# Kernel optimization log

Measured on AMD Instinct MI355X. Metric: run time of the kernel, lower is better.

## Reference

```python
import jax, jax.numpy as jnp
import numpy as np

B, M, N, Z = 4, 64, 64, 64
IN_DIM, OUT_DIM = 32, 32
MODES1 = MODES2 = MODES3 = 16
HIDDEN = OUT_DIM * 4  # factor=4, n_ff_layers=2
LN_EPS = 1e-5


def setup_inputs() -> dict:
    key = jax.random.key(0)
    ks = jax.random.split(key, 10)
    # xavier-normal-ish scale for (in, out, modes, 2) fourier weights
    fscale = np.sqrt(2.0 / (IN_DIM + OUT_DIM))
    x = jax.random.normal(ks[0], (B, M, N, Z, IN_DIM), dtype=jnp.float32)
    wx = jax.random.normal(ks[1], (IN_DIM, OUT_DIM, MODES1, 2), dtype=jnp.float32) * fscale
    wy = jax.random.normal(ks[2], (IN_DIM, OUT_DIM, MODES2, 2), dtype=jnp.float32) * fscale
    wz = jax.random.normal(ks[3], (IN_DIM, OUT_DIM, MODES3, 2), dtype=jnp.float32) * fscale
    # FeedForward: Linear(OUT_DIM, HIDDEN) + ReLU, then Linear(HIDDEN, OUT_DIM) + LayerNorm
    w0 = jax.random.normal(ks[4], (OUT_DIM, HIDDEN), dtype=jnp.float32) * np.sqrt(1.0 / OUT_DIM)
    b0 = jnp.zeros((HIDDEN,), dtype=jnp.float32)
    w1 = jax.random.normal(ks[5], (HIDDEN, OUT_DIM), dtype=jnp.float32) * np.sqrt(1.0 / HIDDEN)
    b1 = jnp.zeros((OUT_DIM,), dtype=jnp.float32)
    ln_g = jnp.ones((OUT_DIM,), dtype=jnp.float32)
    ln_b = jnp.zeros((OUT_DIM,), dtype=jnp.float32)
    return {"x": x, "wx": wx, "wy": wy, "wz": wz,
            "w0": w0, "b0": b0, "w1": w1, "b1": b1,
            "ln_g": ln_g, "ln_b": ln_b}


def _as_complex(w):
    return w[..., 0] + 1j * w[..., 1]


def _forward_fourier(x, wx, wy, wz):
    # x: [b, m, n, z, i] -> [b, i, m, n, z]
    xt = jnp.transpose(x, (0, 4, 1, 2, 3))
    # --- axis M (dim 2) ---
    ftx = jnp.fft.rfft(xt, axis=2, norm='ortho')  # [b, i, M//2+1, n, z] complex
    ox = jnp.einsum('bixyz,iox->boxyz', ftx[:, :, :MODES1], _as_complex(wx))
    ox = jnp.pad(ox, ((0, 0), (0, 0), (0, M // 2 + 1 - MODES1), (0, 0), (0, 0)))
    xx = jnp.fft.irfft(ox, n=M, axis=2, norm='ortho')
    # --- axis N (dim 3) ---
    fty = jnp.fft.rfft(xt, axis=3, norm='ortho')
    oy = jnp.einsum('bixyz,ioy->boxyz', fty[:, :, :, :MODES2], _as_complex(wy))
    oy = jnp.pad(oy, ((0, 0), (0, 0), (0, 0), (0, N // 2 + 1 - MODES2), (0, 0)))
    xy = jnp.fft.irfft(oy, n=N, axis=3, norm='ortho')
    # --- axis Z (dim 4) ---
    ftz = jnp.fft.rfft(xt, axis=4, norm='ortho')
    oz = jnp.einsum('bixyz,ioz->boxyz', ftz[:, :, :, :, :MODES3], _as_complex(wz))
    oz = jnp.pad(oz, ((0, 0), (0, 0), (0, 0), (0, 0), (0, Z // 2 + 1 - MODES3)))
    xz = jnp.fft.irfft(oz, n=Z, axis=4, norm='ortho')
    out = xx + xy + xz  # [b, o, m, n, z]
    return jnp.transpose(out, (0, 2, 3, 4, 1))  # [b, m, n, z, o]


def reference(x, wx, wy, wz, w0, b0, w1, b1, ln_g, ln_b):
    s = _forward_fourier(x, wx, wy, wz)
    h = jax.nn.relu(s @ w0 + b0)
    y = h @ w1 + b1
    mu = jnp.mean(y, axis=-1, keepdims=True)
    var = jnp.mean((y - mu) ** 2, axis=-1, keepdims=True)
    y = (y - mu) * jax.lax.rsqrt(var + LN_EPS) * ln_g + ln_b
    return y
```

## Files before the change

### kernel.cpp

```cpp
#include <hip/hip_runtime.h>
#include <math.h>

typedef __attribute__((ext_vector_type(8))) short short8v;
typedef __attribute__((ext_vector_type(4))) float float4v;

constexpr float THETA = 6.28318530717958647692f / 64.0f;

constexpr int S_B = 64 * 64 * 64 * 32;
constexpr int S_M = 64 * 64 * 32;
constexpr int S_N = 64 * 32;
constexpr int S_Z = 32;

__device__ __forceinline__ unsigned short f2bf(float f) {
    unsigned int u = __builtin_bit_cast(unsigned int, f);
    u += 0x7FFFu + ((u >> 16) & 1u);
    return (unsigned short)(u >> 16);
}
__device__ __forceinline__ float bf2f(unsigned int h) {
    return __builtin_bit_cast(float, h << 16);
}

constexpr int WS_TF = 98304, WS_TI = 100352, WS_TOTAL = 102400;

__global__ __launch_bounds__(256)
void setup_frags(const float* __restrict__ wx, const float* __restrict__ wy,
                 const float* __restrict__ wz, unsigned short* __restrict__ W)
{
    int f0 = (blockIdx.x * 256 + threadIdx.x) * 4;
#pragma unroll
    for (int u = 0; u < 4; ++u) {
        int f = f0 + u;
        if (f >= WS_TOTAL) continue;
        unsigned short v;
        if (f < WS_TF) {
            int ax = f >> 15, rem = f & 32767;
            int k = rem >> 11;
            int rem2 = rem & 2047;
            int wt = rem2 >> 10, rt = (rem2 >> 9) & 1, l = (rem2 >> 3) & 63, e = rem2 & 7;
            int o = 16 * rt + (l & 15), i = 8 * (l >> 4) + e;
            const float* w = (ax == 0) ? wx : ((ax == 1) ? wy : wz);
            v = f2bf(w[((i * 32 + o) * 16 + k) * 2 + wt]);
        } else if (f < WS_TI) {
            int rem = f - WS_TF;
            int jt = rem >> 10, s = (rem >> 9) & 1, l = (rem >> 3) & 63, e = rem & 7;
            int kk = l & 15, m = 32 * s + 8 * (l >> 4) + e;
            int jm = (kk * m) & 63;
            float ang = THETA * (float)jm;
            v = f2bf(jt == 0 ? cosf(ang) : sinf(ang));
        } else {
            int rem = f - WS_TI;
            int mt = rem >> 9, l = (rem >> 3) & 63, e = rem & 7;
            int mp = 16 * mt + (l & 15), r = 8 * (l >> 4) + e;
            int k = r & 15;
            float sk = (k == 0) ? (1.0f / 64.0f) : (2.0f / 64.0f);
            int jm = (k * mp) & 63;
            float ang = THETA * (float)jm;
            v = f2bf(r < 16 ? sk * cosf(ang) : -sk * sinf(ang));
        }
        W[f] = v;
    }
}

constexpr int AB_SHORTS = 4096;
__device__ __forceinline__ int ab4(int t, int k, int line, int i) {
    return ((((t * 16 + k) * 4 + line) * 64) + i * 2) ^ (((line ^ k) & 7) << 4);
}
constexpr int P_LS = 1288;
constexpr int P_SHORTS = 4 * P_LS;
__device__ __forceinline__ int p4(int line, int o, int r) {
    return line * P_LS + o * 40 + r;
}

template <int STRIDE>
__device__ __forceinline__ void stageF1(const float* __restrict__ x, long bs,
                                        const unsigned short* __restrict__ tf,
                                        unsigned short* __restrict__ AB,
                                        int lane, int line)
{
    const int gq = lane >> 4, c = lane & 15;
    short8v tfB[2][2];
#pragma unroll
    for (int jt = 0; jt < 2; ++jt)
#pragma unroll
        for (int s = 0; s < 2; ++s)
            tfB[jt][s] = *reinterpret_cast<const short8v*>(tf + ((jt * 2 + s) * 64 + lane) * 8);

    float4v acc[2][2];
#pragma unroll
    for (int rt = 0; rt < 2; ++rt)
#pragma unroll
        for (int jt = 0; jt < 2; ++jt)
            acc[rt][jt] = float4v{0.f, 0.f, 0.f, 0.f};

#pragma unroll
    for (int rt = 0; rt < 2; ++rt) {
        const float* xp = x + bs + 16 * rt + c;
#pragma unroll
        for (int s = 0; s < 2; ++s) {
            short8v a;
#pragma unroll
            for (int e = 0; e < 8; ++e)
                a[e] = (short)f2bf(xp[(long)(32 * s + 8 * gq + e) * STRIDE]);
            acc[rt][0] = __builtin_amdgcn_mfma_f32_16x16x32_bf16(a, tfB[0][s], acc[rt][0], 0, 0, 0);
            acc[rt][1] = __builtin_amdgcn_mfma_f32_16x16x32_bf16(a, tfB[1][s], acc[rt][1], 0, 0, 0);
        }
    }
#pragma unroll
    for (int rt = 0; rt < 2; ++rt)
#pragma unroll
        for (int jt = 0; jt < 2; ++jt) {
            unsigned int lo = (unsigned int)f2bf(acc[rt][jt][0]) | ((unsigned int)f2bf(acc[rt][jt][1]) << 16);
            unsigned int hi = (unsigned int)f2bf(acc[rt][jt][2]) | ((unsigned int)f2bf(acc[rt][jt][3]) << 16);
            *reinterpret_cast<uint2*>(reinterpret_cast<char*>(AB) + ab4(jt, c, line, 16 * rt + 4 * gq)) =
                make_uint2(lo, hi);
        }
}

__device__ __forceinline__ void stageMx4(const unsigned short* __restrict__ wf,
                                         const unsigned short* __restrict__ AB,
                                         unsigned short* __restrict__ P,
                                         int lane, int wave)
{
    const int gq = lane >> 4, c = lane & 15;
    const int t2 = wave >> 1, rt = wave & 1, lc = c & 3;
    for (int k = 0; k < 16; k += 2) {
        float4v acc2[2];
#pragma unroll
        for (int kk = 0; kk < 2; ++kk) {
            const int kc = k + kk;
            short8v aT = *reinterpret_cast<const short8v*>(reinterpret_cast<const char*>(AB) + ab4(0, kc, lc, 8 * gq));
            short8v bT = *reinterpret_cast<const short8v*>(reinterpret_cast<const char*>(AB) + ab4(1, kc, lc, 8 * gq));
            const int w1t = t2 ? 1 : 0, w2t = t2 ? 0 : 1;
            short8v w1 = *reinterpret_cast<const short8v*>(wf + (((kc * 2 + w1t) * 2 + rt) * 64 + lane) * 8);
            short8v w2 = *reinterpret_cast<const short8v*>(wf + (((kc * 2 + w2t) * 2 + rt) * 64 + lane) * 8);
            if (t2) {
                union { short8v s; unsigned int u[4]; } nb;
                nb.s = bT;
#pragma unroll
                for (int j = 0; j < 4; ++j) nb.u[j] ^= 0x80008000u;
                bT = nb.s;
            }
            float4v a2 = float4v{0.f, 0.f, 0.f, 0.f};
            a2 = __builtin_amdgcn_mfma_f32_16x16x32_bf16(w1, aT, a2, 0, 0, 0);
            a2 = __builtin_amdgcn_mfma_f32_16x16x32_bf16(w2, bT, a2, 0, 0, 0);
            acc2[kk] = a2;
        }
        if (c < 4) {
#pragma unroll
            for (int r = 0; r < 4; ++r) {
                unsigned int u = (unsigned int)f2bf(acc2[0][r]) | ((unsigned int)f2bf(acc2[1][r]) << 16);
                *reinterpret_cast<unsigned int*>(&P[p4(c, 16 * rt + 4 * gq + r, 16 * t2 + k)]) = u;
            }
        }
    }
}

template <int AXIS, int MODE>
__global__ __launch_bounds__(256)
void spectral_mfma(const float* __restrict__ x,
                   const unsigned short* __restrict__ wf,
                   const unsigned short* __restrict__ tf,
                   const unsigned short* __restrict__ ti,
                   float* __restrict__ out,
                   unsigned short* __restrict__ pw)
{
    __shared__ __align__(16) unsigned short AB[AB_SHORTS];
    __shared__ __align__(16) unsigned short P[P_SHORTS];

    const int t = threadIdx.x, lane = t & 63, wave = t >> 6;
    const int gq = lane >> 4, c = lane & 15;
    constexpr int stride = (AXIS == 0) ? S_M : S_N;

    const int l = blockIdx.x * 4 + wave;
    const int b = l >> 12, p1 = (l >> 6) & 63, p2 = l & 63;
    const long bs = (AXIS == 0)
        ? (long)b * S_B + (long)p1 * S_N + (long)p2 * S_Z
        : (long)b * S_B + (long)p1 * S_M + (long)p2 * S_Z;

    stageF1<stride>(x, bs, tf, AB, lane, wave);
    __syncthreads();
    stageMx4(wf, AB, P, lane, wave);
    __syncthreads();

    short8v tiB[4];
#pragma unroll
    for (int mt = 0; mt < 4; ++mt)
        tiB[mt] = *reinterpret_cast<const short8v*>(ti + (mt * 64 + lane) * 8);

    short8v pA[2];
    pA[0] = *reinterpret_cast<const short8v*>(&P[p4(wave, c, 8 * gq)]);
    pA[1] = *reinterpret_cast<const short8v*>(&P[p4(wave, 16 + c, 8 * gq)]);

#pragma unroll
    for (int rt = 0; rt < 2; ++rt)
#pragma unroll
        for (int mt = 0; mt < 4; ++mt) {
            float4v acc = float4v{0.f, 0.f, 0.f, 0.f};
            acc = __builtin_amdgcn_mfma_f32_16x16x32_bf16(pA[rt], tiB[mt], acc, 0, 0, 0);
            const long off = bs + (long)(16 * mt + c) * stride + 16 * rt + 4 * gq;
            if (MODE == 0) {
                *reinterpret_cast<float4*>(out + off) = make_float4(acc[0], acc[1], acc[2], acc[3]);
            } else if (MODE == 1) {
                float4 old = *reinterpret_cast<const float4*>(out + off);
                old.x += acc[0]; old.y += acc[1]; old.z += acc[2]; old.w += acc[3];
                *reinterpret_cast<float4*>(out + off) = old;
            } else if (MODE == 2) {
                uint2 pv;
                pv.x = (unsigned int)f2bf(acc[0]) | ((unsigned int)f2bf(acc[1]) << 16);
                pv.y = (unsigned int)f2bf(acc[2]) | ((unsigned int)f2bf(acc[3]) << 16);
                *reinterpret_cast<uint2*>(pw + off) = pv;
            } else {
                uint2 old = *reinterpret_cast<const uint2*>(pw + off);
                const float v0 = bf2f(old.x & 0xffffu) + acc[0];
                const float v1 = bf2f(old.x >> 16)     + acc[1];
                const float v2 = bf2f(old.y & 0xffffu) + acc[2];
                const float v3 = bf2f(old.y >> 16)     + acc[3];
                uint2 pv;
                pv.x = (unsigned int)f2bf(v0) | ((unsigned int)f2bf(v1) << 16);
                pv.y = (unsigned int)f2bf(v2) | ((unsigned int)f2bf(v3) << 16);
                *reinterpret_cast<uint2*>(pw + off) = pv;
            }
        }
}

template <bool BF16P>
__global__ __launch_bounds__(256)
void spectral_fused(const float* __restrict__ x,
                    const unsigned short* __restrict__ wf,
                    const unsigned short* __restrict__ tf,
                    const unsigned short* __restrict__ ti,
                    const float* __restrict__ w0, const float* __restrict__ b0,
                    const float* __restrict__ w1, const float* __restrict__ b1,
                    const float* __restrict__ g,  const float* __restrict__ bb,
                    const void* __restrict__ partial,
                    float* __restrict__ out)
{
    __shared__ __align__(16) unsigned short sm[23584];
    constexpr int OP = 8192, OS = 13344;

    const int t = threadIdx.x, lane = t & 63, wave = t >> 6;
    const int gq = lane >> 4, c = lane & 15;

    const int l = blockIdx.x * 4 + wave;
    const int b = l >> 12, p1 = (l >> 6) & 63, p2 = l & 63;
    const long bs = (long)b * S_B + (long)p1 * S_M + (long)p2 * S_N;

    float b0v[8], b1v[2], gv[2], bvv[2];
#pragma unroll
    for (int n = 0; n < 8; ++n) b0v[n] = b0[n * 16 + c];
#pragma unroll
    for (int n = 0; n < 2; ++n) { b1v[n] = b1[n * 16 + c]; gv[n] = g[n * 16 + c]; bvv[n] = bb[n * 16 + c]; }

    stageF1<S_Z>(x, bs, tf, sm, lane, wave);
    __syncthreads();
    stageMx4(wf, sm, sm + OP, lane, wave);
    __syncthreads();

    for (int s = t; s < 512; s += 256) {
        const int n = s >> 6, ln = s & 63, g2 = ln >> 4, c2 = ln & 15;
        const int kb = n >> 1, nn = n & 1;
        short8v v0, v1;
#pragma unroll
        for (int e = 0; e < 8; ++e) {
            v0[e] = (short)f2bf(w0[(8 * g2 + e) * 128 + n * 16 + c2]);
            v1[e] = (short)f2bf(w1[(32 * kb + 8 * g2 + e) * 32 + nn * 16 + c2]);
        }
        *reinterpret_cast<short8v*>(&sm[s * 8])        = v0;
        *reinterpret_cast<short8v*>(&sm[4096 + s * 8]) = v1;
    }

    short8v tiB[4];
#pragma unroll
    for (int mt = 0; mt < 4; ++mt)
        tiB[mt] = *reinterpret_cast<const short8v*>(ti + (mt * 64 + lane) * 8);

    {
        short8v pA[2];
        pA[0] = *reinterpret_cast<const short8v*>(&sm[OP + p4(wave, c, 8 * gq)]);
        pA[1] = *reinterpret_cast<const short8v*>(&sm[OP + p4(wave, 16 + c, 8 * gq)]);
#pragma unroll
        for (int rt = 0; rt < 2; ++rt)
#pragma unroll
            for (int mt = 0; mt < 4; ++mt) {
                float4v acc = float4v{0.f, 0.f, 0.f, 0.f};
                acc = __builtin_amdgcn_mfma_f32_16x16x32_bf16(pA[rt], tiB[mt], acc, 0, 0, 0);
                const long off = bs + (long)(16 * mt + c) * S_Z + 16 * rt + 4 * gq;
                float v0, v1, v2, v3;
                if (BF16P) {
                    uint2 pv = *reinterpret_cast<const uint2*>((const unsigned short*)partial + off);
                    v0 = bf2f(pv.x & 0xffffu) + acc[0];
                    v1 = bf2f(pv.x >> 16)     + acc[1];
                    v2 = bf2f(pv.y & 0xffffu) + acc[2];
                    v3 = bf2f(pv.y >> 16)     + acc[3];
                } else {
                    float4 old = *reinterpret_cast<const float4*>((const float*)partial + off);
                    v0 = old.x + acc[0]; v1 = old.y + acc[1];
                    v2 = old.z + acc[2]; v3 = old.w + acc[3];
                }
                const int si = OS + (wave * 64 + 16 * mt + c) * 40 + 16 * rt + 4 * gq;
                *reinterpret_cast<unsigned int*>(&sm[si])     = (unsigned int)f2bf(v0) | ((unsigned int)f2bf(v1) << 16);
                *reinterpret_cast<unsigned int*>(&sm[si + 2]) = (unsigned int)f2bf(v2) | ((unsigned int)f2bf(v3) << 16);
            }
    }
    __syncthreads();

    const int Hb = OS + wave * 2560;

    short8v af[4];
#pragma unroll
    for (int f = 0; f < 4; ++f)
        af[f] = *reinterpret_cast<const short8v*>(&sm[OS + (wave * 64 + 16 * f + c) * 40 + 8 * gq]);

    float4v Y[4][2];
#pragma unroll
    for (int f = 0; f < 4; ++f)
#pragma unroll
        for (int n = 0; n < 2; ++n)
            Y[f][n] = float4v{b1v[n], b1v[n], b1v[n], b1v[n]};

#pragma unroll
    for (int kb = 0; kb < 4; ++kb) {
#pragma unroll
        for (int nn = 0; nn < 2; ++nn) {
            const int n = 2 * kb + nn;
            const short8v wv = *reinterpret_cast<const short8v*>(&sm[(n * 64 + lane) * 8]);
#pragma unroll
            for (int f = 0; f < 4; ++f) {
                float4v hacc = float4v{b0v[n], b0v[n], b0v[n], b0v[n]};
                hacc = __builtin_amdgcn_mfma_f32_16x16x32_bf16(af[f], wv, hacc, 0, 0, 0);
#pragma unroll
                for (int r = 0; r < 4; ++r)
                    sm[Hb + (16 * f + 4 * gq + r) * 40 + nn * 16 + c] = f2bf(fmaxf(hacc[r], 0.f));
            }
        }
        const short8v wva = *reinterpret_cast<const short8v*>(&sm[4096 + ((kb * 2 + 0) * 64 + lane) * 8]);
        const short8v wvb = *reinterpret_cast<const short8v*>(&sm[4096 + ((kb * 2 + 1) * 64 + lane) * 8]);
#pragma unroll
        for (int f = 0; f < 4; ++f) {
            const short8v a2 = *reinterpret_cast<const short8v*>(&sm[Hb + (16 * f + c) * 40 + 8 * gq]);
            Y[f][0] = __builtin_amdgcn_mfma_f32_16x16x32_bf16(a2, wva, Y[f][0], 0, 0, 0);
            Y[f][1] = __builtin_amdgcn_mfma_f32_16x16x32_bf16(a2, wvb, Y[f][1], 0, 0, 0);
        }
    }

#pragma unroll
    for (int f = 0; f < 4; ++f) {
        float smv[4], sq[4];
#pragma unroll
        for (int r = 0; r < 4; ++r) {
            const float v0 = Y[f][0][r], v1 = Y[f][1][r];
            smv[r] = v0 + v1;
            sq[r]  = v0 * v0 + v1 * v1;
        }
#pragma unroll
        for (int mask = 1; mask <= 8; mask <<= 1) {
#pragma unroll
            for (int r = 0; r < 4; ++r) {
                smv[r] += __shfl_xor(smv[r], mask);
                sq[r]  += __shfl_xor(sq[r], mask);
            }
        }
#pragma unroll
        for (int r = 0; r < 4; ++r) {
            const float mu = smv[r] * (1.0f / 32.0f);
            const float var = sq[r] * (1.0f / 32.0f) - mu * mu;
            const float rs = rsqrtf(var + 1e-5f);
            float* op = out + bs + (long)(16 * f + 4 * gq + r) * 32;
            op[c]      = (Y[f][0][r] - mu) * rs * gv[0] + bvv[0];
            op[16 + c] = (Y[f][1][r] - mu) * rs * gv[1] + bvv[1];
        }
    }
}

extern "C" void kernel_launch(void* const* d_in, const int* in_sizes, int n_in,
                              void* d_out, int out_size, void* d_ws, size_t ws_size,
                              hipStream_t stream)
{
    const float* x    = (const float*)d_in[0];
    const float* wx   = (const float*)d_in[1];
    const float* wy   = (const float*)d_in[2];
    const float* wz   = (const float*)d_in[3];
    const float* w0   = (const float*)d_in[4];
    const float* b0   = (const float*)d_in[5];
    const float* w1   = (const float*)d_in[6];
    const float* b1   = (const float*)d_in[7];
    const float* ln_g = (const float*)d_in[8];
    const float* ln_b = (const float*)d_in[9];
    float* out = (float*)d_out;

    unsigned short* wsf = (unsigned short*)d_ws;

    const size_t PART_OFF   = 262144;
    const size_t PART_BYTES = (size_t)33554432 * 2;
    const bool bf16p = ws_size >= PART_OFF + PART_BYTES;
    unsigned short* pw = (unsigned short*)((char*)d_ws + PART_OFF);

    setup_frags<<<100, 256, 0, stream>>>(wx, wy, wz, wsf);

    if (bf16p) {
        spectral_mfma<0, 2><<<4096, 256, 0, stream>>>(x, wsf + 0 * 32768, wsf + WS_TF, wsf + WS_TI, out, pw);
        spectral_mfma<1, 3><<<4096, 256, 0, stream>>>(x, wsf + 1 * 32768, wsf + WS_TF, wsf + WS_TI, out, pw);
        spectral_fused<true><<<4096, 256, 0, stream>>>(x, wsf + 2 * 32768, wsf + WS_TF, wsf + WS_TI,
                                                       w0, b0, w1, b1, ln_g, ln_b, pw, out);
    } else {
        spectral_mfma<0, 0><<<4096, 256, 0, stream>>>(x, wsf + 0 * 32768, wsf + WS_TF, wsf + WS_TI, out, pw);
        spectral_mfma<1, 1><<<4096, 256, 0, stream>>>(x, wsf + 1 * 32768, wsf + WS_TF, wsf + WS_TI, out, pw);
        spectral_fused<false><<<4096, 256, 0, stream>>>(x, wsf + 2 * 32768, wsf + WS_TF, wsf + WS_TI,
                                                        w0, b0, w1, b1, ln_g, ln_b, out, out);
    }
}
```

Baseline: 229.1 us.

## Merge X and Y spectral passes into one launch with separate bf16 partial buffers

Adds a combined spectral_xy kernel that runs the M-axis and N-axis spectral passes as one 8192-block launch. Each pass writes its own bf16 partial buffer, which removes the read-modify-write accumulation of the second pass and lets both passes run concurrently. The fused Z/FFN kernel then reads and sums both partials. Smaller changes: bf16 conversion now uses the native __bf16 cast, and the first FFN matmul is transposed so each lane stores a packed uint2 instead of four scalar shared-memory writes. The new path needs twice the workspace for partials and falls back to the old paths otherwise.

```diff
diff --git a/kernel.cpp b/kernel.cpp
--- a/kernel.cpp
+++ b/kernel.cpp
@@ -12,9 +12,11 @@
 constexpr int S_Z = 32;
 
 __device__ __forceinline__ unsigned short f2bf(float f) {
-    unsigned int u = __builtin_bit_cast(unsigned int, f);
-    u += 0x7FFFu + ((u >> 16) & 1u);
-    return (unsigned short)(u >> 16);
+    __bf16 h = (__bf16)f;
+    return __builtin_bit_cast(unsigned short, h);
+}
+__device__ __forceinline__ unsigned int pkbf(float lo, float hi) {
+    return (unsigned int)f2bf(lo) | ((unsigned int)f2bf(hi) << 16);
 }
 __device__ __forceinline__ float bf2f(unsigned int h) {
     return __builtin_bit_cast(float, h << 16);
@@ -109,10 +111,8 @@
     for (int rt = 0; rt < 2; ++rt)
 #pragma unroll
         for (int jt = 0; jt < 2; ++jt) {
-            unsigned int lo = (unsigned int)f2bf(acc[rt][jt][0]) | ((unsigned int)f2bf(acc[rt][jt][1]) << 16);
-            unsigned int hi = (unsigned int)f2bf(acc[rt][jt][2]) | ((unsigned int)f2bf(acc[rt][jt][3]) << 16);
             *reinterpret_cast<uint2*>(reinterpret_cast<char*>(AB) + ab4(jt, c, line, 16 * rt + 4 * gq)) =
-                make_uint2(lo, hi);
+                make_uint2(pkbf(acc[rt][jt][0], acc[rt][jt][1]), pkbf(acc[rt][jt][2], acc[rt][jt][3]));
         }
 }
 
@@ -148,10 +148,72 @@
         if (c < 4) {
 #pragma unroll
             for (int r = 0; r < 4; ++r) {
-                unsigned int u = (unsigned int)f2bf(acc2[0][r]) | ((unsigned int)f2bf(acc2[1][r]) << 16);
-                *reinterpret_cast<unsigned int*>(&P[p4(c, 16 * rt + 4 * gq + r, 16 * t2 + k)]) = u;
-            }
-        }
+                *reinterpret_cast<unsigned int*>(&P[p4(c, 16 * rt + 4 * gq + r, 16 * t2 + k)]) =
+                    pkbf(acc2[0][r], acc2[1][r]);
+            }
+        }
+    }
+}
+
+template <int AXIS>
+__device__ __forceinline__ void spectral_body(const float* __restrict__ x,
+                                              const unsigned short* __restrict__ wf,
+                                              const unsigned short* __restrict__ tf,
+                                              const unsigned short* __restrict__ ti,
+                                              unsigned short* __restrict__ pw,
+                                              unsigned short* __restrict__ AB,
+                                              unsigned short* __restrict__ P,
+                                              int l, int lane, int wave)
+{
+    constexpr int stride = (AXIS == 0) ? S_M : S_N;
+    const int b = l >> 12, p1 = (l >> 6) & 63, p2 = l & 63;
+    const long bs = (AXIS == 0)
+        ? (long)b * S_B + (long)p1 * S_N + (long)p2 * S_Z
+        : (long)b * S_B + (long)p1 * S_M + (long)p2 * S_Z;
+    const int gq = lane >> 4, c = lane & 15;
+
+    stageF1<stride>(x, bs, tf, AB, lane, wave);
+    __syncthreads();
+    stageMx4(wf, AB, P, lane, wave);
+    __syncthreads();
+
+    short8v tiB[4];
+#pragma unroll
+    for (int mt = 0; mt < 4; ++mt)
+        tiB[mt] = *reinterpret_cast<const short8v*>(ti + (mt * 64 + lane) * 8);
+
+    short8v pA[2];
+    pA[0] = *reinterpret_cast<const short8v*>(&P[p4(wave, c, 8 * gq)]);
+    pA[1] = *reinterpret_cast<const short8v*>(&P[p4(wave, 16 + c, 8 * gq)]);
+
+#pragma unroll
+    for (int rt = 0; rt < 2; ++rt)
+#pragma unroll
+        for (int mt = 0; mt < 4; ++mt) {
+            float4v acc = float4v{0.f, 0.f, 0.f, 0.f};
+            acc = __builtin_amdgcn_mfma_f32_16x16x32_bf16(pA[rt], tiB[mt], acc, 0, 0, 0);
+            const long off = bs + (long)(16 * mt + c) * stride + 16 * rt + 4 * gq;
+            *reinterpret_cast<uint2*>(pw + off) =
+                make_uint2(pkbf(acc[0], acc[1]), pkbf(acc[2], acc[3]));
+        }
+}
+
+__global__ __launch_bounds__(256)
+void spectral_xy(const float* __restrict__ x,
+                 const unsigned short* __restrict__ wf0,
+                 const unsigned short* __restrict__ wf1,
+                 const unsigned short* __restrict__ tf,
+                 const unsigned short* __restrict__ ti,
+                 unsigned short* __restrict__ pw1,
+                 unsigned short* __restrict__ pw2)
+{
+    __shared__ __align__(16) unsigned short AB[AB_SHORTS];
+    __shared__ __align__(16) unsigned short P[P_SHORTS];
+    const int t = threadIdx.x, lane = t & 63, wave = t >> 6;
+    if (blockIdx.x < 4096) {
+        spectral_body<0>(x, wf0, tf, ti, pw1, AB, P, blockIdx.x * 4 + wave, lane, wave);
+    } else {
+        spectral_body<1>(x, wf1, tf, ti, pw2, AB, P, (blockIdx.x - 4096) * 4 + wave, lane, wave);
     }
 }
 
@@ -205,25 +267,21 @@
                 old.x += acc[0]; old.y += acc[1]; old.z += acc[2]; old.w += acc[3];
                 *reinterpret_cast<float4*>(out + off) = old;
             } else if (MODE == 2) {
-                uint2 pv;
-                pv.x = (unsigned int)f2bf(acc[0]) | ((unsigned int)f2bf(acc[1]) << 16);
-                pv.y = (unsigned int)f2bf(acc[2]) | ((unsigned int)f2bf(acc[3]) << 16);
-                *reinterpret_cast<uint2*>(pw + off) = pv;
+                *reinterpret_cast<uint2*>(pw + off) =
+                    make_uint2(pkbf(acc[0], acc[1]), pkbf(acc[2], acc[3]));
             } else {
                 uint2 old = *reinterpret_cast<const uint2*>(pw + off);
                 const float v0 = bf2f(old.x & 0xffffu) + acc[0];
                 const float v1 = bf2f(old.x >> 16)     + acc[1];
                 const float v2 = bf2f(old.y & 0xffffu) + acc[2];
                 const float v3 = bf2f(old.y >> 16)     + acc[3];
-                uint2 pv;
-                pv.x = (unsigned int)f2bf(v0) | ((unsigned int)f2bf(v1) << 16);
-                pv.y = (unsigned int)f2bf(v2) | ((unsigned int)f2bf(v3) << 16);
-                *reinterpret_cast<uint2*>(pw + off) = pv;
-            }
-        }
-}
-
-template <bool BF16P>
+                *reinterpret_cast<uint2*>(pw + off) =
+                    make_uint2(pkbf(v0, v1), pkbf(v2, v3));
+            }
+        }
+}
+
+template <int NPART>
 __global__ __launch_bounds__(256)
 void spectral_fused(const float* __restrict__ x,
                     const unsigned short* __restrict__ wf,
@@ -232,7 +290,9 @@
                     const float* __restrict__ w0, const float* __restrict__ b0,
                     const float* __restrict__ w1, const float* __restrict__ b1,
                     const float* __restrict__ g,  const float* __restrict__ bb,
-                    const void* __restrict__ partial,
+                    const unsigned short* __restrict__ pw1,
+                    const unsigned short* __restrict__ pw2,
+                    const float* __restrict__ pf32,
                     float* __restrict__ out)
 {
     __shared__ __align__(16) unsigned short sm[23584];
@@ -245,9 +305,11 @@
     const int b = l >> 12, p1 = (l >> 6) & 63, p2 = l & 63;
     const long bs = (long)b * S_B + (long)p1 * S_M + (long)p2 * S_N;
 
-    float b0v[8], b1v[2], gv[2], bvv[2];
-#pragma unroll
-    for (int n = 0; n < 8; ++n) b0v[n] = b0[n * 16 + c];
+    float4 b0q[8];
+#pragma unroll
+    for (int n = 0; n < 8; ++n)
+        b0q[n] = *reinterpret_cast<const float4*>(b0 + 16 * n + 4 * gq);
+    float b1v[2], gv[2], bvv[2];
 #pragma unroll
     for (int n = 0; n < 2; ++n) { b1v[n] = b1[n * 16 + c]; gv[n] = g[n * 16 + c]; bvv[n] = bb[n * 16 + c]; }
 
@@ -286,20 +348,26 @@
                 acc = __builtin_amdgcn_mfma_f32_16x16x32_bf16(pA[rt], tiB[mt], acc, 0, 0, 0);
                 const long off = bs + (long)(16 * mt + c) * S_Z + 16 * rt + 4 * gq;
                 float v0, v1, v2, v3;
-                if (BF16P) {
-                    uint2 pv = *reinterpret_cast<const uint2*>((const unsigned short*)partial + off);
+                if (NPART == 0) {
+                    float4 old = *reinterpret_cast<const float4*>(pf32 + off);
+                    v0 = old.x + acc[0]; v1 = old.y + acc[1];
+                    v2 = old.z + acc[2]; v3 = old.w + acc[3];
+                } else {
+                    uint2 pv = *reinterpret_cast<const uint2*>(pw1 + off);
                     v0 = bf2f(pv.x & 0xffffu) + acc[0];
                     v1 = bf2f(pv.x >> 16)     + acc[1];
                     v2 = bf2f(pv.y & 0xffffu) + acc[2];
                     v3 = bf2f(pv.y >> 16)     + acc[3];
-                } else {
-                    float4 old = *reinterpret_cast<const float4*>((const float*)partial + off);
-                    v0 = old.x + acc[0]; v1 = old.y + acc[1];
-                    v2 = old.z + acc[2]; v3 = old.w + acc[3];
+                    if (NPART == 2) {
+                        uint2 qv = *reinterpret_cast<const uint2*>(pw2 + off);
+                        v0 += bf2f(qv.x & 0xffffu);
+                        v1 += bf2f(qv.x >> 16);
+                        v2 += bf2f(qv.y & 0xffffu);
+                        v3 += bf2f(qv.y >> 16);
+                    }
                 }
                 const int si = OS + (wave * 64 + 16 * mt + c) * 40 + 16 * rt + 4 * gq;
-                *reinterpret_cast<unsigned int*>(&sm[si])     = (unsigned int)f2bf(v0) | ((unsigned int)f2bf(v1) << 16);
-                *reinterpret_cast<unsigned int*>(&sm[si + 2]) = (unsigned int)f2bf(v2) | ((unsigned int)f2bf(v3) << 16);
+                *reinterpret_cast<uint2*>(&sm[si]) = make_uint2(pkbf(v0, v1), pkbf(v2, v3));
             }
     }
     __syncthreads();
@@ -326,11 +394,12 @@
             const short8v wv = *reinterpret_cast<const short8v*>(&sm[(n * 64 + lane) * 8]);
 #pragma unroll
             for (int f = 0; f < 4; ++f) {
-                float4v hacc = float4v{b0v[n], b0v[n], b0v[n], b0v[n]};
-                hacc = __builtin_amdgcn_mfma_f32_16x16x32_bf16(af[f], wv, hacc, 0, 0, 0);
-#pragma unroll
-                for (int r = 0; r < 4; ++r)
-                    sm[Hb + (16 * f + 4 * gq + r) * 40 + nn * 16 + c] = f2bf(fmaxf(hacc[r], 0.f));
+                float4v hacc = float4v{b0q[n].x, b0q[n].y, b0q[n].z, b0q[n].w};
+                hacc = __builtin_amdgcn_mfma_f32_16x16x32_bf16(wv, af[f], hacc, 0, 0, 0);
+                const float h0 = fmaxf(hacc[0], 0.f), h1 = fmaxf(hacc[1], 0.f);
+                const float h2 = fmaxf(hacc[2], 0.f), h3 = fmaxf(hacc[3], 0.f);
+                *reinterpret_cast<uint2*>(&sm[Hb + (16 * f + c) * 40 + 16 * nn + 4 * gq]) =
+                    make_uint2(pkbf(h0, h1), pkbf(h2, h3));
             }
         }
         const short8v wva = *reinterpret_cast<const short8v*>(&sm[4096 + ((kb * 2 + 0) * 64 + lane) * 8]);
@@ -392,20 +461,27 @@
 
     const size_t PART_OFF   = 262144;
     const size_t PART_BYTES = (size_t)33554432 * 2;
-    const bool bf16p = ws_size >= PART_OFF + PART_BYTES;
-    unsigned short* pw = (unsigned short*)((char*)d_ws + PART_OFF);
+    unsigned short* pw1 = (unsigned short*)((char*)d_ws + PART_OFF);
+    unsigned short* pw2 = (unsigned short*)((char*)d_ws + PART_OFF + PART_BYTES);
+    const int tier = (ws_size >= PART_OFF + 2 * PART_BYTES) ? 2
+                   : (ws_size >= PART_OFF + PART_BYTES)     ? 1 : 0;
 
     setup_frags<<<100, 256, 0, stream>>>(wx, wy, wz, wsf);
 
-    if (bf16p) {
-        spectral_mfma<0, 2><<<4096, 256, 0, stream>>>(x, wsf + 0 * 32768, wsf + WS_TF, wsf + WS_TI, out, pw);
-        spectral_mfma<1, 3><<<4096, 256, 0, stream>>>(x, wsf + 1 * 32768, wsf + WS_TF, wsf + WS_TI, out, pw);
-        spectral_fused<true><<<4096, 256, 0, stream>>>(x, wsf + 2 * 32768, wsf + WS_TF, wsf + WS_TI,
-                                                       w0, b0, w1, b1, ln_g, ln_b, pw, out);
+    if (tier == 2) {
+        spectral_xy<<<8192, 256, 0, stream>>>(x, wsf + 0 * 32768, wsf + 1 * 32768,
+                                              wsf + WS_TF, wsf + WS_TI, pw1, pw2);
+        spectral_fused<2><<<4096, 256, 0, stream>>>(x, wsf + 2 * 32768, wsf + WS_TF, wsf + WS_TI,
+                                                    w0, b0, w1, b1, ln_g, ln_b, pw1, pw2, out, out);
+    } else if (tier == 1) {
+        spectral_mfma<0, 2><<<4096, 256, 0, stream>>>(x, wsf + 0 * 32768, wsf + WS_TF, wsf + WS_TI, out, pw1);
+        spectral_mfma<1, 3><<<4096, 256, 0, stream>>>(x, wsf + 1 * 32768, wsf + WS_TF, wsf + WS_TI, out, pw1);
+        spectral_fused<1><<<4096, 256, 0, stream>>>(x, wsf + 2 * 32768, wsf + WS_TF, wsf + WS_TI,
+                                                    w0, b0, w1, b1, ln_g, ln_b, pw1, pw1, out, out);
     } else {
-        spectral_mfma<0, 0><<<4096, 256, 0, stream>>>(x, wsf + 0 * 32768, wsf + WS_TF, wsf + WS_TI, out, pw);
-        spectral_mfma<1, 1><<<4096, 256, 0, stream>>>(x, wsf + 1 * 32768, wsf + WS_TF, wsf + WS_TI, out, pw);
-        spectral_fused<false><<<4096, 256, 0, stream>>>(x, wsf + 2 * 32768, wsf + WS_TF, wsf + WS_TI,
-                                                        w0, b0, w1, b1, ln_g, ln_b, out, out);
-    }
-}
+        spectral_mfma<0, 0><<<4096, 256, 0, stream>>>(x, wsf + 0 * 32768, wsf + WS_TF, wsf + WS_TI, out, pw1);
+        spectral_mfma<1, 1><<<4096, 256, 0, stream>>>(x, wsf + 1 * 32768, wsf + WS_TF, wsf + WS_TI, out, pw1);
+        spectral_fused<0><<<4096, 256, 0, stream>>>(x, wsf + 2 * 32768, wsf + WS_TF, wsf + WS_TI,
+                                                    w0, b0, w1, b1, ln_g, ln_b, pw1, pw1, out, out);
+    }
+}
```

After: 225.9 us. About the same (-1.4%).
